# Performance work log

Hardware: AMD Instinct MI355X
Metric: run time of the kernel (lower is better)

## Reference

```python
import jax, jax.numpy as jnp
import numpy as np

L = 8          # fixed number of instance labels (0 = background), all assumed present
DV = 0.5       # delta_v
DD = 1.5       # delta_d
LOSS_WEIGHT = 1.0


def _safe_norm(x, axis):
    sq = jnp.sum(x * x, axis=axis)
    pos = sq > 0
    return jnp.sqrt(jnp.where(pos, sq, 1.0)) * pos.astype(x.dtype)


def _per_image(emb, inst, kern, tmask):
    # emb: [D,H,W], inst: [H,W] int, kern/tmask: [H,W] float
    D, H, W = emb.shape
    HW = H * W
    tm = (tmask > 0.5).astype(inst.dtype)
    kb = (kern > 0.5).astype(inst.dtype)
    inst = inst * tm
    inst_k = (inst * kb).reshape(-1)          # kernel-region labels
    inst_f = inst.reshape(-1)                 # full-region labels
    emb_f = emb.reshape(D, -1).T              # [HW, D]

    # --- generate_coef: first/second occurrence (row-major) of each label ---
    flat = jnp.arange(HW)
    eq = inst_f[None, :] == jnp.arange(L)[:, None]          # [L, HW]
    idxs = jnp.where(eq, flat[None, :], HW)
    first = jnp.min(idxs, axis=1)
    second = jnp.min(jnp.where(idxs == first[:, None], HW, idxs), axis=1)
    first = jnp.minimum(first, HW - 1)
    second = jnp.minimum(second, HW - 1)
    r0, c0 = first // W, first % W
    r1, c1 = second // W, second % W
    # pos_id = (tmp[0,0], tmp[1,0], tmp[0,-1], tmp[1,-1]) as in the source
    pos = jnp.stack([r0, r1, c0, c1], axis=1).astype(jnp.float32)  # [L,4]
    diag = jnp.sqrt(jnp.float32(H * H + W * W))
    coef_diag = jnp.exp(jnp.sqrt((pos[:, 0] - pos[:, 2]) ** 2 +
                                 (pos[:, 1] - pos[:, 3]) ** 2) / diag / 2.0)
    zmask = (jnp.arange(L) > 0).astype(jnp.float32)          # skip label 0
    coef_diag = coef_diag * zmask
    s = pos[:, 0] + pos[:, 2]
    t = pos[:, 1] + pos[:, 3]
    dp = jnp.sqrt((s[:, None] - s[None, :]) ** 2 + (t[:, None] - t[None, :]) ** 2)
    coef_off = 1.0 - 20.0 * jnp.exp(-4.0 - 2.5 * dp / diag)
    eye = jnp.eye(L, dtype=bool)
    coef = jnp.where(eye, coef_diag[:, None], coef_off)
    coef = coef * zmask[:, None] * zmask[None, :]

    # --- per-label kernel means (segment mean) ---
    ones = jnp.ones((HW,), jnp.float32)
    cnt_k = jax.ops.segment_sum(ones, inst_k, num_segments=L)
    mean = jax.ops.segment_sum(emb_f, inst_k, num_segments=L)
    mean = mean / jnp.maximum(cnt_k, 1.0)[:, None]           # [L, D]
    mean = mean * zmask[:, None]

    # --- l_agg: per-pixel distance to own-label mean, segment-mean per label ---
    mean_px = mean[inst_f]                                   # [HW, D] gather
    dist = _safe_norm(emb_f - mean_px, axis=1)
    cd_px = coef_diag[inst_f]
    val = jnp.log(jax.nn.relu(cd_px * dist - DV) ** 2 + 1.0)
    cnt = jax.ops.segment_sum(ones, inst_f, num_segments=L)
    l_agg_per = jax.ops.segment_sum(val, inst_f, num_segments=L) / jnp.maximum(cnt, 1.0)
    l_agg = jnp.mean(l_agg_per[1:])

    # --- l_dis: coefficient-weighted pairwise hinge between means ---
    Dn = _safe_norm(mean[:, None, :] - mean[None, :, :], axis=-1)  # [L, L]
    pm = (~eye) & (zmask[:, None] > 0) & (zmask[None, :] > 0)
    vals = jnp.log(jax.nn.relu(2.0 * DD - coef * Dn) ** 2 + 1.0)
    l_dis = jnp.sum(jnp.where(pm, vals, 0.0)) / ((L - 1) * (L - 2))

    # --- l_reg ---
    l_reg = jnp.mean(jnp.log(_safe_norm(mean, axis=1) + 1.0)) * 0.001
    return l_agg + l_dis + l_reg


def reference(emb, instance, kernel, training_mask, bboxes):
    # bboxes is accepted but unused, matching the original forward_single
    loss_batch = jax.vmap(_per_image)(emb, instance, kernel, training_mask)
    return LOSS_WEIGHT * jnp.mean(loss_batch)


def setup_inputs() -> dict:
    key = jax.random.key(0)
    k1, k2, k3, k4, k5 = jax.random.split(key, 5)
    B, D, H, W = 8, 4, 640, 640
    emb = jax.random.normal(k1, (B, D, H, W), dtype=jnp.float32)
    instance = jax.random.randint(k2, (B, H, W), 0, L, dtype=jnp.int32)
    kernel = jax.random.uniform(k3, (B, H, W), dtype=jnp.float32)
    training_mask = jax.random.uniform(k4, (B, H, W), dtype=jnp.float32)
    bboxes = jax.random.uniform(k5, (B, 10, 4), dtype=jnp.float32)
    return {"emb": emb, "instance": instance, "kernel": kernel,
            "training_mask": training_mask, "bboxes": bboxes}
```

## Files before the change

### kernel.cpp

```cpp
#include <hip/hip_runtime.h>

#define B_    8
#define D_    4
#define H_    640
#define W_    640
#define HW_   (H_ * W_)
#define L_    8
#define NL    (L_ - 1)
#define BLOCK 256
#define VITER 4
#define PXB   (BLOCK * 4 * VITER)
#define GRIDX (HW_ / PXB)

__device__ __forceinline__ void gatom_add(float* p, float v) {
    unsafeAtomicAdd(p, v);
}

__global__ void k_init(int* ib) {
    int t = threadIdx.x;
    if (t < 128) ib[t] = HW_;
    ib[128 + t] = 0;
    if (t < 137) ib[384 + t] = 0;
}

__global__ __attribute__((amdgpu_flat_work_group_size(BLOCK, BLOCK),
                          amdgpu_waves_per_eu(4, 4)))
void k_pass1(
        const float* __restrict__ emb, const int* __restrict__ inst,
        const float* __restrict__ kern, const float* __restrict__ tmask,
        int* __restrict__ firstIdx, int* __restrict__ secondIdx,
        int* __restrict__ cntf_i, int* __restrict__ cntk_i,
        float* __restrict__ sumemb, uint2* __restrict__ lblpack) {
    __shared__ int   sCnt[L_];
    __shared__ float sSum[L_ * D_];
    __shared__ int   sM1[L_], sM2[L_];

    const int tid  = threadIdx.x;
    const int lane = tid & 63;
    if (tid < L_) { sCnt[tid] = 0; sM1[tid] = HW_; sM2[tid] = HW_; }
    if (tid < L_ * D_) sSum[tid] = 0.f;
    __syncthreads();

    const int b = blockIdx.y;
    const int blockbase = blockIdx.x * PXB;
    const float* embb = emb + (size_t)b * D_ * HW_;
    const int base = b * HW_;
    const int o0 = blockbase + tid * 4;

    int4 LB[2]; float4 TM[2], KN[2], E0[2], E1[2], E2[2], E3[2];
    {
        LB[0] = *(const int4*)  (inst  + base + o0);
        TM[0] = *(const float4*)(tmask + base + o0);
        KN[0] = *(const float4*)(kern  + base + o0);
        E0[0] = *(const float4*)(embb + 0 * HW_ + o0);
        E1[0] = *(const float4*)(embb + 1 * HW_ + o0);
        E2[0] = *(const float4*)(embb + 2 * HW_ + o0);
        E3[0] = *(const float4*)(embb + 3 * HW_ + o0);
    }

    float sm[NL][D_];
    #pragma unroll
    for (int l = 0; l < NL; ++l)
        #pragma unroll
        for (int d = 0; d < D_; ++d) sm[l][d] = 0.f;
    int bp0 = 0, bp1 = 0, bp2 = 0, km = 0;
    unsigned int lpLo = 0, lpHi = 0;

    #pragma unroll
    for (int it = 0; it < VITER; ++it) {
        const int cur = it & 1, nxt = cur ^ 1;
        if (it + 1 < VITER) {
            const int o = o0 + (it + 1) * (BLOCK * 4);
            LB[nxt] = *(const int4*)  (inst  + base + o);
            TM[nxt] = *(const float4*)(tmask + base + o);
            KN[nxt] = *(const float4*)(kern  + base + o);
            E0[nxt] = *(const float4*)(embb + 0 * HW_ + o);
            E1[nxt] = *(const float4*)(embb + 1 * HW_ + o);
            E2[nxt] = *(const float4*)(embb + 2 * HW_ + o);
            E3[nxt] = *(const float4*)(embb + 3 * HW_ + o);
        }
        const int*   labA = (const int*)&LB[cur];
        const float* tmA  = (const float*)&TM[cur];
        const float* knA  = (const float*)&KN[cur];
        const float* e0A  = (const float*)&E0[cur];
        const float* e1A  = (const float*)&E1[cur];
        const float* e2A  = (const float*)&E2[cur];
        const float* e3A  = (const float*)&E3[cur];

        #pragma unroll
        for (int c = 0; c < 4; ++c) {
            const int px = it * 4 + c;
            const int lf  = (tmA[c] > 0.5f) ? labA[c] : 0;
            const bool kb = (knA[c] > 0.5f);
            const int lfk = kb ? lf : 0;
            bp0 |= (lf & 1) << px;
            bp1 |= ((lf >> 1) & 1) << px;
            bp2 |= ((lf >> 2) & 1) << px;
            km  |= (kb ? 1 : 0) << px;
            if (px < 8) lpLo |= (unsigned int)lf << (4 * px);
            else        lpHi |= (unsigned int)lf << (4 * (px - 8));
            #pragma unroll
            for (int l = 1; l < L_; ++l) {
                const float mk = (lfk == l) ? 1.0f : 0.0f;
                sm[l - 1][0] += mk * e0A[c];
                sm[l - 1][1] += mk * e1A[c];
                sm[l - 1][2] += mk * e2A[c];
                sm[l - 1][3] += mk * e3A[c];
            }
        }
    }

    lblpack[(size_t)(b * GRIDX + blockIdx.x) * BLOCK + tid] = make_uint2(lpLo, lpHi);

    const int nb0 = ~bp0, nb1 = ~bp1, nb2 = ~bp2;
    int cnt[NL], m1[NL], m2[NL];
    #pragma unroll
    for (int l = 1; l < L_; ++l) {
        const int k = l - 1;
        int h = ((l & 1) ? bp0 : nb0) & ((l & 2) ? bp1 : nb1) & ((l & 4) ? bp2 : nb2);
        h &= 0xFFFF;
        cnt[k] = (__popc(h) << 16) | __popc(h & km);
        const int h2 = h & (h - 1);
        const int p1 = __ffs(h) - 1;
        const int p2 = __ffs(h2) - 1;
        m1[k] = h  ? (o0 + (p1 >> 2) * (BLOCK * 4) + (p1 & 3)) : HW_;
        m2[k] = h2 ? (o0 + (p2 >> 2) * (BLOCK * 4) + (p2 & 3)) : HW_;
    }

    #pragma unroll
    for (int l = 0; l < NL; ++l) {
        #pragma unroll
        for (int off = 32; off > 0; off >>= 1) {
            cnt[l]   += __shfl_down(cnt[l], off);
            sm[l][0] += __shfl_down(sm[l][0], off);
            sm[l][1] += __shfl_down(sm[l][1], off);
            sm[l][2] += __shfl_down(sm[l][2], off);
            sm[l][3] += __shfl_down(sm[l][3], off);
            int o1 = __shfl_down(m1[l], off);
            int o2 = __shfl_down(m2[l], off);
            m2[l] = min(min(m2[l], o2), max(m1[l], o1));
            m1[l] = min(m1[l], o1);
        }
    }
    if (lane == 0) {
        #pragma unroll
        for (int l = 0; l < NL; ++l) {
            atomicAdd(&sCnt[l + 1], cnt[l]);
            #pragma unroll
            for (int d = 0; d < D_; ++d) atomicAdd(&sSum[(l + 1) * D_ + d], sm[l][d]);
            int old = atomicMin(&sM1[l + 1], m1[l]);
            atomicMin(&sM2[l + 1], max(old, m1[l]));
            atomicMin(&sM2[l + 1], m2[l]);
        }
    }
    __syncthreads();

    if (tid >= 1 && tid < L_) {
        const int pc = sCnt[tid];
        atomicAdd(&cntf_i[b * L_ + tid], pc >> 16);
        atomicAdd(&cntk_i[b * L_ + tid], pc & 0xFFFF);
        int old = atomicMin(&firstIdx[b * L_ + tid], sM1[tid]);
        atomicMin(&secondIdx[b * L_ + tid], max(old, sM1[tid]));
        atomicMin(&secondIdx[b * L_ + tid], sM2[tid]);
    }
    if (tid >= D_ && tid < L_ * D_)
        gatom_add(&sumemb[b * L_ * D_ + tid], sSum[tid]);
}

__global__ __attribute__((amdgpu_flat_work_group_size(BLOCK, BLOCK),
                          amdgpu_waves_per_eu(4, 4)))
void k_pass3(
        const float* __restrict__ emb, const uint2* __restrict__ lblpack,
        const int* __restrict__ firstIdx, const int* __restrict__ secondIdx,
        const int* __restrict__ cntk_i, const int* __restrict__ cntf_i,
        const float* __restrict__ sumemb, float* __restrict__ sumvalb) {
    __shared__ float4 sMean[L_];
    __shared__ float  sCd[L_], sInv[L_];
    __shared__ float  sAcc;

    const int tid = threadIdx.x;
    const int b   = blockIdx.y;

    if (tid < L_) {
        float4 mu = {0.f, 0.f, 0.f, 0.f};
        float cd = 0.f, inv = 0.f;
        if (tid > 0) {
            const float invk = 1.0f / fmaxf((float)cntk_i[b * L_ + tid], 1.0f);
            mu.x = sumemb[b * L_ * D_ + tid * D_ + 0] * invk;
            mu.y = sumemb[b * L_ * D_ + tid * D_ + 1] * invk;
            mu.z = sumemb[b * L_ * D_ + tid * D_ + 2] * invk;
            mu.w = sumemb[b * L_ * D_ + tid * D_ + 3] * invk;
            const float diag = sqrtf((float)(H_ * H_ + W_ * W_));
            int f = min(firstIdx[b * L_ + tid],  HW_ - 1);
            int s = min(secondIdx[b * L_ + tid], HW_ - 1);
            float r0 = (float)(f / W_), c0 = (float)(f % W_);
            float r1 = (float)(s / W_), c1 = (float)(s % W_);
            cd = __expf(sqrtf((r0 - c0) * (r0 - c0) + (r1 - c1) * (r1 - c1))
                        / diag * 0.5f);
            inv = 1.0f / fmaxf((float)cntf_i[b * L_ + tid], 1.0f);
        }
        sMean[tid] = mu; sCd[tid] = cd; sInv[tid] = inv;
        if (tid == 0) sAcc = 0.f;
    }
    __syncthreads();

    const int blockbase = blockIdx.x * PXB;
    const float* embb = emb + (size_t)b * D_ * HW_;
    const int o0 = blockbase + tid * 4;

    const uint2 lp = lblpack[(size_t)(b * GRIDX + blockIdx.x) * BLOCK + tid];
    float4 E[VITER][D_];
    #pragma unroll
    for (int it = 0; it < VITER; ++it)
        #pragma unroll
        for (int d = 0; d < D_; ++d)
            E[it][d] = *(const float4*)(embb + d * HW_ + o0 + it * (BLOCK * 4));

    float acc = 0.f;
    #pragma unroll
    for (int it = 0; it < VITER; ++it) {
        const float* e0A = (const float*)&E[it][0];
        const float* e1A = (const float*)&E[it][1];
        const float* e2A = (const float*)&E[it][2];
        const float* e3A = (const float*)&E[it][3];
        #pragma unroll
        for (int c = 0; c < 4; ++c) {
            const int px = it * 4 + c;
            const int lf = (int)(((px < 8) ? (lp.x >> (4 * px))
                                           : (lp.y >> (4 * (px - 8)))) & 7u);
            const float4 mu = sMean[lf];
            float dx = e0A[c] - mu.x, dy = e1A[c] - mu.y;
            float dz = e2A[c] - mu.z, dw = e3A[c] - mu.w;
            float d2 = dx * dx + dy * dy + dz * dz + dw * dw;
            float x  = fmaxf(sCd[lf] * sqrtf(d2) - 0.5f, 0.0f);
            acc += __logf(x * x + 1.0f) * sInv[lf];
        }
    }

    #pragma unroll
    for (int off = 32; off > 0; off >>= 1)
        acc += __shfl_down(acc, off);
    if ((tid & 63) == 0) atomicAdd(&sAcc, acc);
    __syncthreads();
    if (tid == 0) gatom_add(&sumvalb[b], sAcc);
}

__global__ __launch_bounds__(512) void k_final(
        const int* __restrict__ firstIdx, const int* __restrict__ secondIdx,
        const int* __restrict__ cntk_i, const float* __restrict__ sumemb,
        const float* __restrict__ sumvalb, float* __restrict__ out) {
    __shared__ float sWave[8];
    const int tid = threadIdx.x;
    const int b = tid >> 6, ij = tid & 63, i = ij >> 3, j = ij & 7;
    const float diag = sqrtf((float)(H_ * H_ + W_ * W_));

    float mi[D_], mj[D_];
    {
        float ci = 1.0f / fmaxf((float)cntk_i[b * L_ + i], 1.0f);
        float cj = 1.0f / fmaxf((float)cntk_i[b * L_ + j], 1.0f);
        #pragma unroll
        for (int d = 0; d < D_; ++d) {
            mi[d] = (i > 0) ? sumemb[(b * L_ + i) * D_ + d] * ci : 0.0f;
            mj[d] = (j > 0) ? sumemb[(b * L_ + j) * D_ + d] * cj : 0.0f;
        }
    }

    float contrib = 0.0f;
    if (j == 0) {
        float d2 = 0.f;
        #pragma unroll
        for (int d = 0; d < D_; ++d) d2 += mi[d] * mi[d];
        float n = (d2 > 0.f) ? sqrtf(d2) : 0.f;
        contrib += __logf(n + 1.0f) * (0.001f / (float)L_);
    }
    if (i == 0 && j == 1)
        contrib += sumvalb[b] * (1.0f / (float)NL);
    if (i >= 1 && j >= 1 && i != j) {
        float d2 = 0.f;
        #pragma unroll
        for (int d = 0; d < D_; ++d) {
            float df = mi[d] - mj[d];
            d2 += df * df;
        }
        float Dn = (d2 > 0.f) ? sqrtf(d2) : 0.f;
        int fi = min(firstIdx[b * L_ + i],  HW_ - 1);
        int si = min(secondIdx[b * L_ + i], HW_ - 1);
        int fj = min(firstIdx[b * L_ + j],  HW_ - 1);
        int sj = min(secondIdx[b * L_ + j], HW_ - 1);
        float ssi = (float)(fi / W_) + (float)(fi % W_);
        float tti = (float)(si / W_) + (float)(si % W_);
        float ssj = (float)(fj / W_) + (float)(fj % W_);
        float ttj = (float)(sj / W_) + (float)(sj % W_);
        float dx = ssi - ssj, dy = tti - ttj;
        float dp = sqrtf(dx * dx + dy * dy);
        float coef = 1.0f - 20.0f * __expf(-4.0f - 2.5f * dp / diag);
        float x = fmaxf(3.0f - coef * Dn, 0.0f);
        contrib += __logf(x * x + 1.0f) * (1.0f / 42.0f);
    }

    #pragma unroll
    for (int off = 32; off > 0; off >>= 1)
        contrib += __shfl_down(contrib, off);
    if ((tid & 63) == 0) sWave[tid >> 6] = contrib;
    __syncthreads();
    if (tid == 0) {
        float t = 0.f;
        #pragma unroll
        for (int w = 0; w < 8; ++w) t += sWave[w];
        out[0] = t * (1.0f / (float)B_);
    }
}

extern "C" void kernel_launch(void* const* d_in, const int* in_sizes, int n_in,
                              void* d_out, int out_size, void* d_ws, size_t ws_size,
                              hipStream_t stream) {
    const float* emb   = (const float*)d_in[0];
    const int*   inst  = (const int*)  d_in[1];
    const float* kern  = (const float*)d_in[2];
    const float* tmask = (const float*)d_in[3];

    int*   ib        = (int*)d_ws;
    int*   firstIdx  = ib;
    int*   secondIdx = ib + 64;
    int*   cntf_i    = ib + 128;
    int*   cntk_i    = ib + 192;
    float* sumemb    = (float*)(ib + 256);
    float* sumvalb   = (float*)(ib + 512);
    uint2* lblpack   = (uint2*)(ib + 1024);
    float* out       = (float*)d_out;

    dim3 grid(GRIDX, B_);

    k_init <<<1, 256, 0, stream>>>(ib);
    k_pass1<<<grid, BLOCK, 0, stream>>>(emb, inst, kern, tmask,
                                        firstIdx, secondIdx, cntf_i, cntk_i,
                                        sumemb, lblpack);
    k_pass3<<<grid, BLOCK, 0, stream>>>(emb, lblpack, firstIdx, secondIdx,
                                        cntk_i, cntf_i, sumemb, sumvalb);
    k_final<<<1, 512, 0, stream>>>(firstIdx, secondIdx, cntk_i,
                                   sumemb, sumvalb, out);
}
```

Before: 149.9 us.

## Halve pixels per thread, issue all loads up front, pack labels into one word

Each thread now handles 8 pixels instead of 16, which doubles the grid. All global loads are issued before the compute, separated by a scheduling barrier, instead of being double-buffered. The per-thread label pack shrinks from uint2 to a single 32-bit word, and the bitmask logic is narrowed to match. Launch bounds change from waves_per_eu(4,4) to __launch_bounds__(BLOCK,2). The aim is more memory parallelism through more blocks and more loads in flight per thread, at the cost of more blocks and more atomic traffic in the reductions.

After: 169.7 us. 1.13x slower.

```diff
diff --git a/kernel.cpp b/kernel.cpp
--- a/kernel.cpp
+++ b/kernel.cpp
@@ -8,7 +8,7 @@
 #define L_    8
 #define NL    (L_ - 1)
 #define BLOCK 256
-#define VITER 4
+#define VITER 2
 #define PXB   (BLOCK * 4 * VITER)
 #define GRIDX (HW_ / PXB)
 
@@ -23,14 +23,12 @@
     if (t < 137) ib[384 + t] = 0;
 }
 
-__global__ __attribute__((amdgpu_flat_work_group_size(BLOCK, BLOCK),
-                          amdgpu_waves_per_eu(4, 4)))
-void k_pass1(
+__global__ __launch_bounds__(BLOCK, 2) void k_pass1(
         const float* __restrict__ emb, const int* __restrict__ inst,
         const float* __restrict__ kern, const float* __restrict__ tmask,
         int* __restrict__ firstIdx, int* __restrict__ secondIdx,
         int* __restrict__ cntf_i, int* __restrict__ cntk_i,
-        float* __restrict__ sumemb, uint2* __restrict__ lblpack) {
+        float* __restrict__ sumemb, unsigned int* __restrict__ lblpack) {
     __shared__ int   sCnt[L_];
     __shared__ float sSum[L_ * D_];
     __shared__ int   sM1[L_], sM2[L_];
@@ -46,17 +44,23 @@
     const float* embb = emb + (size_t)b * D_ * HW_;
     const int base = b * HW_;
     const int o0 = blockbase + tid * 4;
-
-    int4 LB[2]; float4 TM[2], KN[2], E0[2], E1[2], E2[2], E3[2];
-    {
-        LB[0] = *(const int4*)  (inst  + base + o0);
-        TM[0] = *(const float4*)(tmask + base + o0);
-        KN[0] = *(const float4*)(kern  + base + o0);
-        E0[0] = *(const float4*)(embb + 0 * HW_ + o0);
-        E1[0] = *(const float4*)(embb + 1 * HW_ + o0);
-        E2[0] = *(const float4*)(embb + 2 * HW_ + o0);
-        E3[0] = *(const float4*)(embb + 3 * HW_ + o0);
-    }
+    const int o1 = o0 + BLOCK * 4;
+
+    const int4   lb0 = *(const int4*)  (inst  + base + o0);
+    const int4   lb1 = *(const int4*)  (inst  + base + o1);
+    const float4 tm0 = *(const float4*)(tmask + base + o0);
+    const float4 tm1 = *(const float4*)(tmask + base + o1);
+    const float4 kn0 = *(const float4*)(kern  + base + o0);
+    const float4 kn1 = *(const float4*)(kern  + base + o1);
+    const float4 e00 = *(const float4*)(embb + 0 * HW_ + o0);
+    const float4 e01 = *(const float4*)(embb + 1 * HW_ + o0);
+    const float4 e02 = *(const float4*)(embb + 2 * HW_ + o0);
+    const float4 e03 = *(const float4*)(embb + 3 * HW_ + o0);
+    const float4 e10 = *(const float4*)(embb + 0 * HW_ + o1);
+    const float4 e11 = *(const float4*)(embb + 1 * HW_ + o1);
+    const float4 e12 = *(const float4*)(embb + 2 * HW_ + o1);
+    const float4 e13 = *(const float4*)(embb + 3 * HW_ + o1);
+    __builtin_amdgcn_sched_barrier(0);
 
     float sm[NL][D_];
     #pragma unroll
@@ -64,32 +68,19 @@
         #pragma unroll
         for (int d = 0; d < D_; ++d) sm[l][d] = 0.f;
     int bp0 = 0, bp1 = 0, bp2 = 0, km = 0;
-    unsigned int lpLo = 0, lpHi = 0;
-
-    #pragma unroll
-    for (int it = 0; it < VITER; ++it) {
-        const int cur = it & 1, nxt = cur ^ 1;
-        if (it + 1 < VITER) {
-            const int o = o0 + (it + 1) * (BLOCK * 4);
-            LB[nxt] = *(const int4*)  (inst  + base + o);
-            TM[nxt] = *(const float4*)(tmask + base + o);
-            KN[nxt] = *(const float4*)(kern  + base + o);
-            E0[nxt] = *(const float4*)(embb + 0 * HW_ + o);
-            E1[nxt] = *(const float4*)(embb + 1 * HW_ + o);
-            E2[nxt] = *(const float4*)(embb + 2 * HW_ + o);
-            E3[nxt] = *(const float4*)(embb + 3 * HW_ + o);
-        }
-        const int*   labA = (const int*)&LB[cur];
-        const float* tmA  = (const float*)&TM[cur];
-        const float* knA  = (const float*)&KN[cur];
-        const float* e0A  = (const float*)&E0[cur];
-        const float* e1A  = (const float*)&E1[cur];
-        const float* e2A  = (const float*)&E2[cur];
-        const float* e3A  = (const float*)&E3[cur];
-
+    unsigned int lp = 0;
+
+    {
+        const int*   labA = (const int*)&lb0;
+        const float* tmA  = (const float*)&tm0;
+        const float* knA  = (const float*)&kn0;
+        const float* e0A  = (const float*)&e00;
+        const float* e1A  = (const float*)&e01;
+        const float* e2A  = (const float*)&e02;
+        const float* e3A  = (const float*)&e03;
         #pragma unroll
         for (int c = 0; c < 4; ++c) {
-            const int px = it * 4 + c;
+            const int px = c;
             const int lf  = (tmA[c] > 0.5f) ? labA[c] : 0;
             const bool kb = (knA[c] > 0.5f);
             const int lfk = kb ? lf : 0;
@@ -97,8 +88,7 @@
             bp1 |= ((lf >> 1) & 1) << px;
             bp2 |= ((lf >> 2) & 1) << px;
             km  |= (kb ? 1 : 0) << px;
-            if (px < 8) lpLo |= (unsigned int)lf << (4 * px);
-            else        lpHi |= (unsigned int)lf << (4 * (px - 8));
+            lp  |= (unsigned int)lf << (4 * px);
             #pragma unroll
             for (int l = 1; l < L_; ++l) {
                 const float mk = (lfk == l) ? 1.0f : 0.0f;
@@ -109,8 +99,37 @@
             }
         }
     }
-
-    lblpack[(size_t)(b * GRIDX + blockIdx.x) * BLOCK + tid] = make_uint2(lpLo, lpHi);
+    {
+        const int*   labA = (const int*)&lb1;
+        const float* tmA  = (const float*)&tm1;
+        const float* knA  = (const float*)&kn1;
+        const float* e0A  = (const float*)&e10;
+        const float* e1A  = (const float*)&e11;
+        const float* e2A  = (const float*)&e12;
+        const float* e3A  = (const float*)&e13;
+        #pragma unroll
+        for (int c = 0; c < 4; ++c) {
+            const int px = 4 + c;
+            const int lf  = (tmA[c] > 0.5f) ? labA[c] : 0;
+            const bool kb = (knA[c] > 0.5f);
+            const int lfk = kb ? lf : 0;
+            bp0 |= (lf & 1) << px;
+            bp1 |= ((lf >> 1) & 1) << px;
+            bp2 |= ((lf >> 2) & 1) << px;
+            km  |= (kb ? 1 : 0) << px;
+            lp  |= (unsigned int)lf << (4 * px);
+            #pragma unroll
+            for (int l = 1; l < L_; ++l) {
+                const float mk = (lfk == l) ? 1.0f : 0.0f;
+                sm[l - 1][0] += mk * e0A[c];
+                sm[l - 1][1] += mk * e1A[c];
+                sm[l - 1][2] += mk * e2A[c];
+                sm[l - 1][3] += mk * e3A[c];
+            }
+        }
+    }
+
+    lblpack[(size_t)(b * GRIDX + blockIdx.x) * BLOCK + tid] = lp;
 
     const int nb0 = ~bp0, nb1 = ~bp1, nb2 = ~bp2;
     int cnt[NL], m1[NL], m2[NL];
@@ -118,7 +137,7 @@
     for (int l = 1; l < L_; ++l) {
         const int k = l - 1;
         int h = ((l & 1) ? bp0 : nb0) & ((l & 2) ? bp1 : nb1) & ((l & 4) ? bp2 : nb2);
-        h &= 0xFFFF;
+        h &= 0xFF;
         cnt[k] = (__popc(h) << 16) | __popc(h & km);
         const int h2 = h & (h - 1);
         const int p1 = __ffs(h) - 1;
@@ -136,10 +155,10 @@
             sm[l][1] += __shfl_down(sm[l][1], off);
             sm[l][2] += __shfl_down(sm[l][2], off);
             sm[l][3] += __shfl_down(sm[l][3], off);
-            int o1 = __shfl_down(m1[l], off);
-            int o2 = __shfl_down(m2[l], off);
-            m2[l] = min(min(m2[l], o2), max(m1[l], o1));
-            m1[l] = min(m1[l], o1);
+            int o1v = __shfl_down(m1[l], off);
+            int o2v = __shfl_down(m2[l], off);
+            m2[l] = min(min(m2[l], o2v), max(m1[l], o1v));
+            m1[l] = min(m1[l], o1v);
         }
     }
     if (lane == 0) {
@@ -167,10 +186,8 @@
         gatom_add(&sumemb[b * L_ * D_ + tid], sSum[tid]);
 }
 
-__global__ __attribute__((amdgpu_flat_work_group_size(BLOCK, BLOCK),
-                          amdgpu_waves_per_eu(4, 4)))
-void k_pass3(
-        const float* __restrict__ emb, const uint2* __restrict__ lblpack,
+__global__ __launch_bounds__(BLOCK, 2) void k_pass3(
+        const float* __restrict__ emb, const unsigned int* __restrict__ lblpack,
         const int* __restrict__ firstIdx, const int* __restrict__ secondIdx,
         const int* __restrict__ cntk_i, const int* __restrict__ cntf_i,
         const float* __restrict__ sumemb, float* __restrict__ sumvalb) {
@@ -207,27 +224,44 @@
     const int blockbase = blockIdx.x * PXB;
     const float* embb = emb + (size_t)b * D_ * HW_;
     const int o0 = blockbase + tid * 4;
-
-    const uint2 lp = lblpack[(size_t)(b * GRIDX + blockIdx.x) * BLOCK + tid];
-    float4 E[VITER][D_];
-    #pragma unroll
-    for (int it = 0; it < VITER; ++it)
-        #pragma unroll
-        for (int d = 0; d < D_; ++d)
-            E[it][d] = *(const float4*)(embb + d * HW_ + o0 + it * (BLOCK * 4));
+    const int o1 = o0 + BLOCK * 4;
+
+    const unsigned int lp = lblpack[(size_t)(b * GRIDX + blockIdx.x) * BLOCK + tid];
+    const float4 e00 = *(const float4*)(embb + 0 * HW_ + o0);
+    const float4 e01 = *(const float4*)(embb + 1 * HW_ + o0);
+    const float4 e02 = *(const float4*)(embb + 2 * HW_ + o0);
+    const float4 e03 = *(const float4*)(embb + 3 * HW_ + o0);
+    const float4 e10 = *(const float4*)(embb + 0 * HW_ + o1);
+    const float4 e11 = *(const float4*)(embb + 1 * HW_ + o1);
+    const float4 e12 = *(const float4*)(embb + 2 * HW_ + o1);
+    const float4 e13 = *(const float4*)(embb + 3 * HW_ + o1);
+    __builtin_amdgcn_sched_barrier(0);
 
     float acc = 0.f;
-    #pragma unroll
-    for (int it = 0; it < VITER; ++it) {
-        const float* e0A = (const float*)&E[it][0];
-        const float* e1A = (const float*)&E[it][1];
-        const float* e2A = (const float*)&E[it][2];
-        const float* e3A = (const float*)&E[it][3];
+    {
+        const float* e0A = (const float*)&e00;
+        const float* e1A = (const float*)&e01;
+        const float* e2A = (const float*)&e02;
+        const float* e3A = (const float*)&e03;
         #pragma unroll
         for (int c = 0; c < 4; ++c) {
-            const int px = it * 4 + c;
-            const int lf = (int)(((px < 8) ? (lp.x >> (4 * px))
-                                           : (lp.y >> (4 * (px - 8)))) & 7u);
+            const int lf = (int)((lp >> (4 * c)) & 7u);
+            const float4 mu = sMean[lf];
+            float dx = e0A[c] - mu.x, dy = e1A[c] - mu.y;
+            float dz = e2A[c] - mu.z, dw = e3A[c] - mu.w;
+            float d2 = dx * dx + dy * dy + dz * dz + dw * dw;
+            float x  = fmaxf(sCd[lf] * sqrtf(d2) - 0.5f, 0.0f);
+            acc += __logf(x * x + 1.0f) * sInv[lf];
+        }
+    }
+    {
+        const float* e0A = (const float*)&e10;
+        const float* e1A = (const float*)&e11;
+        const float* e2A = (const float*)&e12;
+        const float* e3A = (const float*)&e13;
+        #pragma unroll
+        for (int c = 0; c < 4; ++c) {
+            const int lf = (int)((lp >> (4 * (4 + c))) & 7u);
             const float4 mu = sMean[lf];
             float dx = e0A[c] - mu.x, dy = e1A[c] - mu.y;
             float dz = e2A[c] - mu.z, dw = e3A[c] - mu.w;
@@ -319,15 +353,15 @@
     const float* kern  = (const float*)d_in[2];
     const float* tmask = (const float*)d_in[3];
 
-    int*   ib        = (int*)d_ws;
-    int*   firstIdx  = ib;
-    int*   secondIdx = ib + 64;
-    int*   cntf_i    = ib + 128;
-    int*   cntk_i    = ib + 192;
-    float* sumemb    = (float*)(ib + 256);
-    float* sumvalb   = (float*)(ib + 512);
-    uint2* lblpack   = (uint2*)(ib + 1024);
-    float* out       = (float*)d_out;
+    int*          ib        = (int*)d_ws;
+    int*          firstIdx  = ib;
+    int*          secondIdx = ib + 64;
+    int*          cntf_i    = ib + 128;
+    int*          cntk_i    = ib + 192;
+    float*        sumemb    = (float*)(ib + 256);
+    float*        sumvalb   = (float*)(ib + 512);
+    unsigned int* lblpack   = (unsigned int*)(ib + 1024);
+    float*        out       = (float*)d_out;
 
     dim3 grid(GRIDX, B_);
 
```
